# Performance work log

Hardware: AMD Instinct MI355X
Metric: run time of the kernel (lower is better)

The kernel has to match this reference:

```python
import jax, jax.numpy as jnp
import numpy as np

N_NODES = 100000
N_EDGES = 300000
HID = 256
N0, N1, N2 = 40000, 30000, 30000
D0, D1, D2 = 512, 256, 128


def setup_inputs() -> dict:
    key = jax.random.key(0)
    ks = jax.random.split(key, 14)
    s = 0.05  # init scale
    return {
        "feat0": jax.random.normal(ks[0], (N0, D0), jnp.float32),
        "feat1": jax.random.normal(ks[1], (N1, D1), jnp.float32),
        "feat2": jax.random.normal(ks[2], (N2, D2), jnp.float32),
        # per-type Linear(in_dim, HID) params (torch Linear: y = x @ W.T + b)
        "fc_w0": jax.random.normal(ks[3], (HID, D0), jnp.float32) * s,
        "fc_b0": jnp.zeros((HID,), jnp.float32),
        "fc_w1": jax.random.normal(ks[4], (HID, D1), jnp.float32) * s,
        "fc_b1": jnp.zeros((HID,), jnp.float32),
        "fc_w2": jax.random.normal(ks[5], (HID, D2), jnp.float32) * s,
        "fc_b2": jnp.zeros((HID,), jnp.float32),
        # GraphConv 1: weight=False, bias=True
        "gc1_bias": jnp.zeros((HID,), jnp.float32),
        # GraphConv 2: weight (in,out) + bias (DGL convention: feat @ W)
        "gc2_weight": jax.random.normal(ks[6], (HID, HID), jnp.float32) * s,
        "gc2_bias": jnp.zeros((HID,), jnp.float32),
        "semantic_weight": jax.random.normal(ks[7], (1, 5), jnp.float32),
        "src": jax.random.randint(ks[8], (N_EDGES,), 0, N_NODES, jnp.int64),
        "dst": jax.random.randint(ks[9], (N_EDGES,), 0, N_NODES, jnp.int64),
    }


def reference(feat0, feat1, feat2, fc_w0, fc_b0, fc_w1, fc_b1, fc_w2, fc_b2,
              gc1_bias, gc2_weight, gc2_bias, semantic_weight, src, dst):
    # per-type projection then concat along node dim -> [N_NODES, HID]
    h = jnp.concatenate([
        feat0 @ fc_w0.T + fc_b0,
        feat1 @ fc_w1.T + fc_b1,
        feat2 @ fc_w2.T + fc_b2,
    ], axis=0)

    ones = jnp.ones((src.shape[0],), h.dtype)
    deg_out = jnp.maximum(jax.ops.segment_sum(ones, src, num_segments=N_NODES), 1.0)
    deg_in = jnp.maximum(jax.ops.segment_sum(ones, dst, num_segments=N_NODES), 1.0)
    norm_out = jax.lax.rsqrt(deg_out)[:, None]  # D_out^{-1/2}
    norm_in = jax.lax.rsqrt(deg_in)[:, None]    # D_in^{-1/2}

    def gconv(x, W, b):
        # DGL GraphConv, norm='both': D_in^{-1/2} A D_out^{-1/2} x W + b, relu
        msg = (x * norm_out)[src]                                  # [E, HID]
        agg = jax.ops.segment_sum(msg, dst, num_segments=N_NODES)  # [N, HID]
        agg = agg * norm_in
        if W is not None:
            agg = agg @ W
        return jax.nn.relu(agg + b)

    # dropout is identity in eval mode
    h = gconv(h, None, gc1_bias)        # layer 0: weight=False
    h = gconv(h, gc2_weight, gc2_bias)  # layer 1
    return h, semantic_weight
```

## Files before the change

kernel.cpp:

```cpp
#include <hip/hip_runtime.h>
#include <cstdint>

#define HID 256
static constexpr int    NNODES = 100000;
static constexpr int    NEDGES = 300000;
static constexpr size_t NH     = (size_t)NNODES * HID;
static constexpr int    SCAN_B = 256;
static constexpr int    NSBLK  = (NNODES + SCAN_B - 1) / SCAN_B;

typedef __attribute__((ext_vector_type(8))) short bf16x8;
typedef __attribute__((ext_vector_type(4))) float f32x4;

__device__ __forceinline__ unsigned short f2bf(float x) {
    unsigned int u = __float_as_uint(x);
    u += 0x7fffu + ((u >> 16) & 1u);
    return (unsigned short)(u >> 16);
}
__device__ __forceinline__ unsigned int pack2(float a, float b) {
    return (unsigned int)f2bf(a) | ((unsigned int)f2bf(b) << 16);
}
__device__ __forceinline__ float bflo(unsigned int u) { return __uint_as_float(u << 16); }
__device__ __forceinline__ float bfhi(unsigned int u) { return __uint_as_float(u & 0xffff0000u); }

__global__ void zero_i32_k(int* __restrict__ p, int n) {
    int i = blockIdx.x * blockDim.x + threadIdx.x;
    if (i < n) p[i] = 0;
}

__global__ void count_deg_k(const int* __restrict__ src, const int* __restrict__ dst,
                            int* __restrict__ degout, int* __restrict__ degin) {
    int e = blockIdx.x * blockDim.x + threadIdx.x;
    if (e < NEDGES) {
        atomicAdd(degout + src[e], 1);
        atomicAdd(degin  + dst[e], 1);
    }
}

__global__ void cvt_weights_k(const float* __restrict__ w0, const float* __restrict__ w1,
                              const float* __restrict__ w2, const float* __restrict__ wg,
                              unsigned short* __restrict__ o0, unsigned short* __restrict__ o1,
                              unsigned short* __restrict__ o2, unsigned short* __restrict__ ogT) {
    int b = blockIdx.x, t = threadIdx.x;
    const float* in; unsigned short* out; int i;
    if (b < 128)      { in = w0; out = o0; i = b * 256 + t; }
    else if (b < 192) { in = w1; out = o1; i = (b - 128) * 256 + t; }
    else if (b < 224) { in = w2; out = o2; i = (b - 192) * 256 + t; }
    else {
        int n = b - 224, k = t;
        ogT[n * 256 + k] = f2bf(wg[k * 256 + n]);
        return;
    }
    float4 v = ((const float4*)in)[i];
    ushort4 w;
    w.x = f2bf(v.x); w.y = f2bf(v.y); w.z = f2bf(v.z); w.w = f2bf(v.w);
    ((ushort4*)out)[i] = w;
}

__global__ void scan_a_k(const int* __restrict__ degin, const int* __restrict__ degout,
                         int* __restrict__ row_off, int* __restrict__ bsums,
                         float* __restrict__ nout, float* __restrict__ nin,
                         const float* __restrict__ sw, float* __restrict__ tail) {
    __shared__ int sm[SCAN_B];
    int t = threadIdx.x;
    int g = blockIdx.x * SCAN_B + t;
    int v = (g < NNODES) ? degin[g] : 0;
    sm[t] = v;
    if (g < NNODES) {
        nout[g] = rsqrtf(fmaxf((float)degout[g], 1.0f));
        nin[g]  = rsqrtf(fmaxf((float)v, 1.0f));
    }
    if (g < 5) tail[g] = sw[g];
    __syncthreads();
#pragma unroll
    for (int off = 1; off < SCAN_B; off <<= 1) {
        int x = (t >= off) ? sm[t - off] : 0;
        __syncthreads();
        sm[t] += x;
        __syncthreads();
    }
    if (g < NNODES) row_off[g] = sm[t] - v;
    if (t == SCAN_B - 1) bsums[blockIdx.x] = sm[t];
}

__global__ void scan_b_k(int* __restrict__ bsums) {
    __shared__ int sm[512];
    int t = threadIdx.x;
    int v = (t < NSBLK) ? bsums[t] : 0;
    sm[t] = v;
    __syncthreads();
#pragma unroll
    for (int off = 1; off < 512; off <<= 1) {
        int x = (t >= off) ? sm[t - off] : 0;
        __syncthreads();
        sm[t] += x;
        __syncthreads();
    }
    if (t < NSBLK) bsums[t] = sm[t] - v;
}

__global__ void scan_c_k(int* __restrict__ row_off, const int* __restrict__ bsums) {
    int g = blockIdx.x * SCAN_B + threadIdx.x;
    if (g < NNODES) row_off[g] += bsums[blockIdx.x];
    if (g == 0) row_off[NNODES] = NEDGES;
}

__global__ void fill_csr_k(const int* __restrict__ src, const int* __restrict__ dst,
                           const int* __restrict__ row_off, int* __restrict__ cursor,
                           int* __restrict__ csr_src) {
    int e = blockIdx.x * blockDim.x + threadIdx.x;
    if (e < NEDGES) {
        int d = dst[e];
        int pos = row_off[d] + atomicAdd(cursor + d, 1);
        csr_src[pos] = src[e];
    }
}

template <int EPI>
__global__ __launch_bounds__(256) void gather_k(
    const unsigned short* __restrict__ h, const int* __restrict__ row_off,
    const int* __restrict__ csr_src, const float* __restrict__ nin,
    const float* __restrict__ bias, void* __restrict__ outv)
{
    int node = blockIdx.x * 4 + (threadIdx.x >> 6);
    if (node >= NNODES) return;
    int lane = threadIdx.x & 63;
    int beg = row_off[node], end = row_off[node + 1];
    float a0 = 0.f, a1 = 0.f, a2 = 0.f, a3 = 0.f;
    for (int base = beg; base < end; base += 64) {
        int cnt = end - base; if (cnt > 64) cnt = 64;
        int idx = csr_src[base + (lane < cnt ? lane : cnt - 1)];
        int j = 0;
        for (; j + 4 <= cnt; j += 4) {
            int s0 = __shfl(idx, j);
            int s1 = __shfl(idx, j + 1);
            int s2 = __shfl(idx, j + 2);
            int s3 = __shfl(idx, j + 3);
            uint2 v0 = *(const uint2*)(h + (size_t)s0 * HID + lane * 4);
            uint2 v1 = *(const uint2*)(h + (size_t)s1 * HID + lane * 4);
            uint2 v2 = *(const uint2*)(h + (size_t)s2 * HID + lane * 4);
            uint2 v3 = *(const uint2*)(h + (size_t)s3 * HID + lane * 4);
            a0 += bflo(v0.x) + bflo(v1.x) + bflo(v2.x) + bflo(v3.x);
            a1 += bfhi(v0.x) + bfhi(v1.x) + bfhi(v2.x) + bfhi(v3.x);
            a2 += bflo(v0.y) + bflo(v1.y) + bflo(v2.y) + bflo(v3.y);
            a3 += bfhi(v0.y) + bfhi(v1.y) + bfhi(v2.y) + bfhi(v3.y);
        }
        for (; j < cnt; ++j) {
            int s = __shfl(idx, j);
            uint2 v = *(const uint2*)(h + (size_t)s * HID + lane * 4);
            a0 += bflo(v.x); a1 += bfhi(v.x);
            a2 += bflo(v.y); a3 += bfhi(v.y);
        }
    }
    if (EPI) {
        float ni = nin[node];
        float4 bb = *(const float4*)(bias + lane * 4);
        float4 o;
        o.x = fmaxf(fmaf(a0, ni, bb.x), 0.f);
        o.y = fmaxf(fmaf(a1, ni, bb.y), 0.f);
        o.z = fmaxf(fmaf(a2, ni, bb.z), 0.f);
        o.w = fmaxf(fmaf(a3, ni, bb.w), 0.f);
        *(float4*)((float*)outv + (size_t)node * HID + lane * 4) = o;
    } else {
        ushort4 o;
        o.x = f2bf(a0); o.y = f2bf(a1); o.z = f2bf(a2); o.w = f2bf(a3);
        *(ushort4*)((unsigned short*)outv + (size_t)node * HID + lane * 4) = o;
    }
}

__global__ __launch_bounds__(512, 4) void proj_mfma_k(
    const float* __restrict__ f0, const float* __restrict__ f1, const float* __restrict__ f2,
    const unsigned short* __restrict__ w0, const unsigned short* __restrict__ w1,
    const unsigned short* __restrict__ w2,
    const float* __restrict__ b0, const float* __restrict__ b1, const float* __restrict__ b2,
    const float* __restrict__ nout, unsigned short* __restrict__ h0)
{
    __shared__ unsigned short As[2][128 * 32];

    int bx = blockIdx.x;
    const float* A; const unsigned short* B; const float* bias; const float* rs;
    unsigned short* C; int M, K;
    if (bx < 313)       { A = f0; B = w0; bias = b0; rs = nout;          C = h0;                          M = 40000; K = 512; }
    else if (bx < 548)  { bx -= 313; A = f1; B = w1; bias = b1; rs = nout + 40000; C = h0 + (size_t)40000 * HID; M = 30000; K = 256; }
    else                { bx -= 548; A = f2; B = w2; bias = b2; rs = nout + 70000; C = h0 + (size_t)70000 * HID; M = 30000; K = 128; }
    const int m0 = bx * 128;

    const int tid  = threadIdx.x;
    const int wid  = tid >> 6;
    const int wm   = wid >> 2;
    const int wn   = wid & 3;
    const int lane = tid & 63;
    const int half = lane >> 4;
    const int l15  = lane & 15;

    f32x4 acc[4][4];
#pragma unroll
    for (int i = 0; i < 4; ++i)
#pragma unroll
        for (int j = 0; j < 4; ++j)
#pragma unroll
            for (int r = 0; r < 4; ++r) acc[i][j][r] = 0.f;

    const int arow = tid >> 2, ac = tid & 3;
    const int aslot = ac ^ ((arow >> 1) & 3);
    int agm = m0 + arow; if (agm > M - 1) agm = M - 1;
    const float* ap = A + (size_t)agm * K + ac * 8;

    const unsigned short* bp = B + (size_t)(wn * 64 + l15 * 4) * K + half * 8;

    const int nT = K >> 5;

    float4 a0E = *(const float4*)ap;
    float4 a1E = *(const float4*)(ap + 4);
    float4 a0O = *(const float4*)(ap + 32);
    float4 a1O = *(const float4*)(ap + 36);
    bf16x8 bcur[4];

#define PROJ_STEP(P, A0, A1)                                                   \
    {                                                                          \
        uint4 u;                                                               \
        u.x = pack2(A0.x, A0.y); u.y = pack2(A0.z, A0.w);                      \
        u.z = pack2(A1.x, A1.y); u.w = pack2(A1.z, A1.w);                      \
        *(uint4*)&As[P][(arow * 4 + aslot) * 8] = u;                           \
        _Pragma("unroll")                                                      \
        for (int j = 0; j < 4; ++j)                                            \
            bcur[j] = *(const bf16x8*)(bp + (size_t)j * K + (tt + P) * 32);    \
        asm volatile("s_waitcnt lgkmcnt(0)" ::: "memory");                     \
        __builtin_amdgcn_s_barrier();                                          \
        __builtin_amdgcn_sched_barrier(0);                                     \
        {                                                                      \
            int tf = tt + P + 2; if (tf > nT - 1) tf = nT - 1;                 \
            const float* pn = ap + tf * 32;                                    \
            A0 = *(const float4*)pn; A1 = *(const float4*)(pn + 4);            \
        }                                                                      \
        bf16x8 af[4];                                                          \
        _Pragma("unroll")                                                      \
        for (int i = 0; i < 4; ++i) {                                          \
            int m = wm * 64 + i * 16 + l15;                                    \
            int ca = half ^ ((m >> 1) & 3);                                    \
            af[i] = *(const bf16x8*)&As[P][(m * 4 + ca) * 8];                  \
        }                                                                      \
        _Pragma("unroll")                                                      \
        for (int i = 0; i < 4; ++i)                                            \
            _Pragma("unroll")                                                  \
            for (int j = 0; j < 4; ++j)                                        \
                acc[i][j] = __builtin_amdgcn_mfma_f32_16x16x32_bf16(           \
                    af[i], bcur[j], acc[i][j], 0, 0, 0);                       \
    }

    for (int tt = 0; tt < nT; tt += 2) {
        PROJ_STEP(0, a0E, a1E)
        PROJ_STEP(1, a0O, a1O)
    }
#undef PROJ_STEP

    float4 bb = *(const float4*)(bias + wn * 64 + l15 * 4);
    const int mwb = m0 + wm * 64;
#pragma unroll
    for (int i = 0; i < 4; ++i) {
        int mb = mwb + i * 16 + half * 4;
        if (mb >= M) continue;
        float4 rv = *(const float4*)(rs + mb);
#pragma unroll
        for (int r = 0; r < 4; ++r) {
            float rsm = (&rv.x)[r];
            ushort4 o;
            o.x = f2bf((acc[i][0][r] + bb.x) * rsm);
            o.y = f2bf((acc[i][1][r] + bb.y) * rsm);
            o.z = f2bf((acc[i][2][r] + bb.z) * rsm);
            o.w = f2bf((acc[i][3][r] + bb.w) * rsm);
            *(ushort4*)&C[(size_t)(mb + r) * HID + wn * 64 + l15 * 4] = o;
        }
    }
}

__global__ __launch_bounds__(512, 4) void mid_mfma_k(
    const unsigned short* __restrict__ agg1, const unsigned short* __restrict__ wT,
    const float* __restrict__ b1, const float* __restrict__ nin,
    const float* __restrict__ nout, unsigned short* __restrict__ h2)
{
    __shared__ unsigned short As[2][128 * 32];

    const int m0   = blockIdx.x * 128;
    const int tid  = threadIdx.x;
    const int wid  = tid >> 6;
    const int wm   = wid >> 2;
    const int wn   = wid & 3;
    const int lane = tid & 63;
    const int half = lane >> 4;
    const int l15  = lane & 15;

    f32x4 acc[4][4];
#pragma unroll
    for (int i = 0; i < 4; ++i)
#pragma unroll
        for (int j = 0; j < 4; ++j)
#pragma unroll
            for (int r = 0; r < 4; ++r) acc[i][j][r] = 0.f;

    const int arow = tid >> 2, ac = tid & 3;
    const int aslot = ac ^ ((arow >> 1) & 3);
    int agm = m0 + arow; if (agm > NNODES - 1) agm = NNODES - 1;
    const float ni = nin[agm], no = nout[agm];
    const unsigned short* ap = agg1 + (size_t)agm * HID + ac * 8;
    const unsigned short* bp = wT + (size_t)(wn * 64 + l15 * 4) * 256 + half * 8;

    uint4  auE = *(const uint4*)ap;
    uint4  auO = *(const uint4*)(ap + 32);
    float4 cE0 = *(const float4*)(b1 + ac * 8);
    float4 cE1 = *(const float4*)(b1 + ac * 8 + 4);
    float4 cO0 = *(const float4*)(b1 + 32 + ac * 8);
    float4 cO1 = *(const float4*)(b1 + 32 + ac * 8 + 4);
    bf16x8 bcur[4];

#define MID_STEP(P, AU, C0, C1)                                                \
    {                                                                          \
        float x0 = fmaxf(fmaf(bflo(AU.x), ni, C0.x), 0.f) * no;                \
        float x1 = fmaxf(fmaf(bfhi(AU.x), ni, C0.y), 0.f) * no;                \
        float x2 = fmaxf(fmaf(bflo(AU.y), ni, C0.z), 0.f) * no;                \
        float x3 = fmaxf(fmaf(bfhi(AU.y), ni, C0.w), 0.f) * no;                \
        float x4 = fmaxf(fmaf(bflo(AU.z), ni, C1.x), 0.f) * no;                \
        float x5 = fmaxf(fmaf(bfhi(AU.z), ni, C1.y), 0.f) * no;                \
        float x6 = fmaxf(fmaf(bflo(AU.w), ni, C1.z), 0.f) * no;                \
        float x7 = fmaxf(fmaf(bfhi(AU.w), ni, C1.w), 0.f) * no;                \
        uint4 o;                                                               \
        o.x = pack2(x0, x1); o.y = pack2(x2, x3);                              \
        o.z = pack2(x4, x5); o.w = pack2(x6, x7);                              \
        *(uint4*)&As[P][(arow * 4 + aslot) * 8] = o;                           \
        _Pragma("unroll")                                                      \
        for (int j = 0; j < 4; ++j)                                            \
            bcur[j] = *(const bf16x8*)(bp + j * 256 + (tt + P) * 32);          \
        asm volatile("s_waitcnt lgkmcnt(0)" ::: "memory");                     \
        __builtin_amdgcn_s_barrier();                                          \
        __builtin_amdgcn_sched_barrier(0);                                     \
        {                                                                      \
            int tf = tt + P + 2; if (tf > 7) tf = 7;                           \
            AU = *(const uint4*)(ap + tf * 32);                                \
            C0 = *(const float4*)(b1 + tf * 32 + ac * 8);                      \
            C1 = *(const float4*)(b1 + tf * 32 + ac * 8 + 4);                  \
        }                                                                      \
        bf16x8 af[4];                                                          \
        _Pragma("unroll")                                                      \
        for (int i = 0; i < 4; ++i) {                                          \
            int m = wm * 64 + i * 16 + l15;                                    \
            int ca = half ^ ((m >> 1) & 3);                                    \
            af[i] = *(const bf16x8*)&As[P][(m * 4 + ca) * 8];                  \
        }                                                                      \
        _Pragma("unroll")                                                      \
        for (int i = 0; i < 4; ++i)                                            \
            _Pragma("unroll")                                                  \
            for (int j = 0; j < 4; ++j)                                        \
                acc[i][j] = __builtin_amdgcn_mfma_f32_16x16x32_bf16(           \
                    af[i], bcur[j], acc[i][j], 0, 0, 0);                       \
    }

    for (int tt = 0; tt < 8; tt += 2) {
        MID_STEP(0, auE, cE0, cE1)
        MID_STEP(1, auO, cO0, cO1)
    }
#undef MID_STEP

    const int mwb = m0 + wm * 64;
#pragma unroll
    for (int i = 0; i < 4; ++i) {
        int mb = mwb + i * 16 + half * 4;
        if (mb >= NNODES) continue;
#pragma unroll
        for (int r = 0; r < 4; ++r) {
            ushort4 o;
            o.x = f2bf(acc[i][0][r]);
            o.y = f2bf(acc[i][1][r]);
            o.z = f2bf(acc[i][2][r]);
            o.w = f2bf(acc[i][3][r]);
            *(ushort4*)&h2[(size_t)(mb + r) * HID + wn * 64 + l15 * 4] = o;
        }
    }
}

extern "C" void kernel_launch(void* const* d_in, const int* in_sizes, int n_in,
                              void* d_out, int out_size, void* d_ws, size_t ws_size,
                              hipStream_t stream)
{
    const float* feat0    = (const float*)d_in[0];
    const float* feat1    = (const float*)d_in[1];
    const float* feat2    = (const float*)d_in[2];
    const float* fc_w0    = (const float*)d_in[3];
    const float* fc_b0    = (const float*)d_in[4];
    const float* fc_w1    = (const float*)d_in[5];
    const float* fc_b1    = (const float*)d_in[6];
    const float* fc_w2    = (const float*)d_in[7];
    const float* fc_b2    = (const float*)d_in[8];
    const float* gc1_bias = (const float*)d_in[9];
    const float* gc2_w    = (const float*)d_in[10];
    const float* gc2_bias = (const float*)d_in[11];
    const float* sw       = (const float*)d_in[12];
    const int*   src      = (const int*)d_in[13];
    const int*   dst      = (const int*)d_in[14];

    unsigned short* h0b  = (unsigned short*)d_ws;
    unsigned short* agg1 = h0b + NH;
    unsigned short* h2b  = h0b;
    unsigned short* w0b  = agg1 + NH;
    unsigned short* w1b  = w0b + 131072;
    unsigned short* w2b  = w1b + 65536;
    unsigned short* w2Tb = w2b + 32768;
    float* nout = (float*)(w2Tb + 65536);
    float* nin  = nout + NNODES;
    int* deg_out = (int*)(nin + NNODES);
    int* deg_in  = deg_out + NNODES;
    int* cursor  = deg_in + NNODES;
    int* row_off = cursor + NNODES;
    int* bsums   = row_off + NNODES + 1;
    int* csr_src = bsums + 512;
    float* out   = (float*)d_out;

    zero_i32_k<<<(3 * NNODES + 255) / 256, 256, 0, stream>>>(deg_out, 3 * NNODES);
    cvt_weights_k<<<480, 256, 0, stream>>>(fc_w0, fc_w1, fc_w2, gc2_w,
                                           w0b, w1b, w2b, w2Tb);
    count_deg_k<<<(NEDGES + 255) / 256, 256, 0, stream>>>(src, dst, deg_out, deg_in);
    scan_a_k<<<NSBLK, SCAN_B, 0, stream>>>(deg_in, deg_out, row_off, bsums,
                                           nout, nin, sw, out + NH);
    scan_b_k<<<1, 512, 0, stream>>>(bsums);
    scan_c_k<<<NSBLK, SCAN_B, 0, stream>>>(row_off, bsums);
    fill_csr_k<<<(NEDGES + 255) / 256, 256, 0, stream>>>(src, dst, row_off, cursor, csr_src);

    proj_mfma_k<<<783, 512, 0, stream>>>(feat0, feat1, feat2, w0b, w1b, w2b,
                                         fc_b0, fc_b1, fc_b2, nout, h0b);

    gather_k<0><<<(NNODES + 3) / 4, 256, 0, stream>>>(h0b, row_off, csr_src,
                                                      nullptr, nullptr, agg1);

    mid_mfma_k<<<782, 512, 0, stream>>>(agg1, w2Tb, gc1_bias, nin, nout, h2b);

    gather_k<1><<<(NNODES + 3) / 4, 256, 0, stream>>>(h2b, row_off, csr_src,
                                                      nin, gc2_bias, out);
}
```

Measured before the change: 441.6 us.

## Shrink GEMM tiles to 64 rows, double-buffer B fragments, persistent gather

```diff
diff --git a/kernel.cpp b/kernel.cpp
--- a/kernel.cpp
+++ b/kernel.cpp
@@ -121,73 +121,83 @@
     const int* __restrict__ csr_src, const float* __restrict__ nin,
     const float* __restrict__ bias, void* __restrict__ outv)
 {
-    int node = blockIdx.x * 4 + (threadIdx.x >> 6);
-    if (node >= NNODES) return;
-    int lane = threadIdx.x & 63;
-    int beg = row_off[node], end = row_off[node + 1];
-    float a0 = 0.f, a1 = 0.f, a2 = 0.f, a3 = 0.f;
-    for (int base = beg; base < end; base += 64) {
-        int cnt = end - base; if (cnt > 64) cnt = 64;
-        int idx = csr_src[base + (lane < cnt ? lane : cnt - 1)];
-        int j = 0;
-        for (; j + 4 <= cnt; j += 4) {
-            int s0 = __shfl(idx, j);
-            int s1 = __shfl(idx, j + 1);
-            int s2 = __shfl(idx, j + 2);
-            int s3 = __shfl(idx, j + 3);
-            uint2 v0 = *(const uint2*)(h + (size_t)s0 * HID + lane * 4);
-            uint2 v1 = *(const uint2*)(h + (size_t)s1 * HID + lane * 4);
-            uint2 v2 = *(const uint2*)(h + (size_t)s2 * HID + lane * 4);
-            uint2 v3 = *(const uint2*)(h + (size_t)s3 * HID + lane * 4);
-            a0 += bflo(v0.x) + bflo(v1.x) + bflo(v2.x) + bflo(v3.x);
-            a1 += bfhi(v0.x) + bfhi(v1.x) + bfhi(v2.x) + bfhi(v3.x);
-            a2 += bflo(v0.y) + bflo(v1.y) + bflo(v2.y) + bflo(v3.y);
-            a3 += bfhi(v0.y) + bfhi(v1.y) + bfhi(v2.y) + bfhi(v3.y);
+    const int nslots = gridDim.x * 4;
+    const int wslot  = blockIdx.x * 4 + (threadIdx.x >> 6);
+    const int lane   = threadIdx.x & 63;
+    const size_t loff = (size_t)lane * 4;
+    float4 bb;
+    if (EPI) bb = *(const float4*)(bias + lane * 4);
+
+    int node = wslot;
+    int beg = 0, end = 0;
+    if (node < NNODES) { beg = row_off[node]; end = row_off[node + 1]; }
+
+    while (node < NNODES) {
+        const int nnode = node + nslots;
+        int nbeg = 0, nend = 0;
+        if (nnode < NNODES) { nbeg = row_off[nnode]; nend = row_off[nnode + 1]; }
+
+        float a0 = 0.f, a1 = 0.f, a2 = 0.f, a3 = 0.f;
+        for (int base = beg; base < end; base += 64) {
+            int cnt = end - base; if (cnt > 64) cnt = 64;
+            int idx = csr_src[base + (lane < cnt ? lane : cnt - 1)];
+            for (int j = 0; j < cnt; j += 8) {
+                uint2 v0 = {0,0}, v1 = {0,0}, v2 = {0,0}, v3 = {0,0};
+                uint2 v4 = {0,0}, v5 = {0,0}, v6 = {0,0}, v7 = {0,0};
+#define GLD(U, VU)                                                              \
+                if (j + U < cnt) {                                              \
+                    int s = __shfl(idx, j + U);                                 \
+                    VU = *(const uint2*)(h + (size_t)s * HID + loff);           \
+                }
+                GLD(0, v0) GLD(1, v1) GLD(2, v2) GLD(3, v3)
+                GLD(4, v4) GLD(5, v5) GLD(6, v6) GLD(7, v7)
+#undef GLD
+                a0 += (bflo(v0.x) + bflo(v1.x)) + (bflo(v2.x) + bflo(v3.x))
+                    + (bflo(v4.x) + bflo(v5.x)) + (bflo(v6.x) + bflo(v7.x));
+                a1 += (bfhi(v0.x) + bfhi(v1.x)) + (bfhi(v2.x) + bfhi(v3.x))
+                    + (bfhi(v4.x) + bfhi(v5.x)) + (bfhi(v6.x) + bfhi(v7.x));
+                a2 += (bflo(v0.y) + bflo(v1.y)) + (bflo(v2.y) + bflo(v3.y))
+                    + (bflo(v4.y) + bflo(v5.y)) + (bflo(v6.y) + bflo(v7.y));
+                a3 += (bfhi(v0.y) + bfhi(v1.y)) + (bfhi(v2.y) + bfhi(v3.y))
+                    + (bfhi(v4.y) + bfhi(v5.y)) + (bfhi(v6.y) + bfhi(v7.y));
+            }
         }
-        for (; j < cnt; ++j) {
-            int s = __shfl(idx, j);
-            uint2 v = *(const uint2*)(h + (size_t)s * HID + lane * 4);
-            a0 += bflo(v.x); a1 += bfhi(v.x);
-            a2 += bflo(v.y); a3 += bfhi(v.y);
+        if (EPI) {
+            float ni = nin[node];
+            float4 o;
+            o.x = fmaxf(fmaf(a0, ni, bb.x), 0.f);
+            o.y = fmaxf(fmaf(a1, ni, bb.y), 0.f);
+            o.z = fmaxf(fmaf(a2, ni, bb.z), 0.f);
+            o.w = fmaxf(fmaf(a3, ni, bb.w), 0.f);
+            *(float4*)((float*)outv + (size_t)node * HID + lane * 4) = o;
+        } else {
+            ushort4 o;
+            o.x = f2bf(a0); o.y = f2bf(a1); o.z = f2bf(a2); o.w = f2bf(a3);
+            *(ushort4*)((unsigned short*)outv + (size_t)node * HID + lane * 4) = o;
         }
-    }
-    if (EPI) {
-        float ni = nin[node];
-        float4 bb = *(const float4*)(bias + lane * 4);
-        float4 o;
-        o.x = fmaxf(fmaf(a0, ni, bb.x), 0.f);
-        o.y = fmaxf(fmaf(a1, ni, bb.y), 0.f);
-        o.z = fmaxf(fmaf(a2, ni, bb.z), 0.f);
-        o.w = fmaxf(fmaf(a3, ni, bb.w), 0.f);
-        *(float4*)((float*)outv + (size_t)node * HID + lane * 4) = o;
-    } else {
-        ushort4 o;
-        o.x = f2bf(a0); o.y = f2bf(a1); o.z = f2bf(a2); o.w = f2bf(a3);
-        *(ushort4*)((unsigned short*)outv + (size_t)node * HID + lane * 4) = o;
-    }
-}
-
-__global__ __launch_bounds__(512, 4) void proj_mfma_k(
+        node = nnode; beg = nbeg; end = nend;
+    }
+}
+
+__global__ __launch_bounds__(256, 3) void proj_mfma_k(
     const float* __restrict__ f0, const float* __restrict__ f1, const float* __restrict__ f2,
     const unsigned short* __restrict__ w0, const unsigned short* __restrict__ w1,
     const unsigned short* __restrict__ w2,
     const float* __restrict__ b0, const float* __restrict__ b1, const float* __restrict__ b2,
     const float* __restrict__ nout, unsigned short* __restrict__ h0)
 {
-    __shared__ unsigned short As[2][128 * 32];
+    __shared__ unsigned short As[2][64 * 32];
 
     int bx = blockIdx.x;
     const float* A; const unsigned short* B; const float* bias; const float* rs;
     unsigned short* C; int M, K;
-    if (bx < 313)       { A = f0; B = w0; bias = b0; rs = nout;          C = h0;                          M = 40000; K = 512; }
-    else if (bx < 548)  { bx -= 313; A = f1; B = w1; bias = b1; rs = nout + 40000; C = h0 + (size_t)40000 * HID; M = 30000; K = 256; }
-    else                { bx -= 548; A = f2; B = w2; bias = b2; rs = nout + 70000; C = h0 + (size_t)70000 * HID; M = 30000; K = 128; }
-    const int m0 = bx * 128;
+    if (bx < 625)       { A = f0; B = w0; bias = b0; rs = nout;          C = h0;                          M = 40000; K = 512; }
+    else if (bx < 1094) { bx -= 625;  A = f1; B = w1; bias = b1; rs = nout + 40000; C = h0 + (size_t)40000 * HID; M = 30000; K = 256; }
+    else                { bx -= 1094; A = f2; B = w2; bias = b2; rs = nout + 70000; C = h0 + (size_t)70000 * HID; M = 30000; K = 128; }
+    const int m0 = bx * 64;
 
     const int tid  = threadIdx.x;
-    const int wid  = tid >> 6;
-    const int wm   = wid >> 2;
-    const int wn   = wid & 3;
+    const int wn   = tid >> 6;
     const int lane = tid & 63;
     const int half = lane >> 4;
     const int l15  = lane & 15;
@@ -209,13 +219,15 @@
 
     const int nT = K >> 5;
 
-    float4 a0E = *(const float4*)ap;
-    float4 a1E = *(const float4*)(ap + 4);
-    float4 a0O = *(const float4*)(ap + 32);
-    float4 a1O = *(const float4*)(ap + 36);
-    bf16x8 bcur[4];
-
-#define PROJ_STEP(P, A0, A1)                                                   \
+    float4 aE0 = *(const float4*)ap;
+    float4 aE1 = *(const float4*)(ap + 4);
+    float4 aO0 = *(const float4*)(ap + 32);
+    float4 aO1 = *(const float4*)(ap + 36);
+    bf16x8 bE[4], bO[4];
+#pragma unroll
+    for (int j = 0; j < 4; ++j) bE[j] = *(const bf16x8*)(bp + (size_t)j * K);
+
+#define PROJ_STEP(P, A0, A1, BC, BN, TB, TF)                                   \
     {                                                                          \
         uint4 u;                                                               \
         u.x = pack2(A0.x, A0.y); u.y = pack2(A0.z, A0.w);                      \
@@ -223,19 +235,19 @@
         *(uint4*)&As[P][(arow * 4 + aslot) * 8] = u;                           \
         _Pragma("unroll")                                                      \
         for (int j = 0; j < 4; ++j)                                            \
-            bcur[j] = *(const bf16x8*)(bp + (size_t)j * K + (tt + P) * 32);    \
+            BN[j] = *(const bf16x8*)(bp + (size_t)j * K + (TB) * 32);          \
         asm volatile("s_waitcnt lgkmcnt(0)" ::: "memory");                     \
         __builtin_amdgcn_s_barrier();                                          \
+        asm volatile("" ::: "memory");                                         \
         __builtin_amdgcn_sched_barrier(0);                                     \
         {                                                                      \
-            int tf = tt + P + 2; if (tf > nT - 1) tf = nT - 1;                 \
-            const float* pn = ap + tf * 32;                                    \
+            const float* pn = ap + (TF) * 32;                                  \
             A0 = *(const float4*)pn; A1 = *(const float4*)(pn + 4);            \
         }                                                                      \
         bf16x8 af[4];                                                          \
         _Pragma("unroll")                                                      \
         for (int i = 0; i < 4; ++i) {                                          \
-            int m = wm * 64 + i * 16 + l15;                                    \
+            int m = i * 16 + l15;                                              \
             int ca = half ^ ((m >> 1) & 3);                                    \
             af[i] = *(const bf16x8*)&As[P][(m * 4 + ca) * 8];                  \
         }                                                                      \
@@ -244,20 +256,23 @@
             _Pragma("unroll")                                                  \
             for (int j = 0; j < 4; ++j)                                        \
                 acc[i][j] = __builtin_amdgcn_mfma_f32_16x16x32_bf16(           \
-                    af[i], bcur[j], acc[i][j], 0, 0, 0);                       \
-    }
-
-    for (int tt = 0; tt < nT; tt += 2) {
-        PROJ_STEP(0, a0E, a1E)
-        PROJ_STEP(1, a0O, a1O)
+                    af[i], BC[j], acc[i][j], 0, 0, 0);                         \
+    }
+
+    for (int t = 0; t < nT; t += 2) {
+        const int tb0 = t + 1;
+        const int tf0 = (t + 2 < nT) ? t + 2 : nT - 1;
+        PROJ_STEP(0, aE0, aE1, bE, bO, tb0, tf0)
+        const int tb1 = (t + 2 < nT) ? t + 2 : nT - 1;
+        const int tf1 = (t + 3 < nT) ? t + 3 : nT - 1;
+        PROJ_STEP(1, aO0, aO1, bO, bE, tb1, tf1)
     }
 #undef PROJ_STEP
 
     float4 bb = *(const float4*)(bias + wn * 64 + l15 * 4);
-    const int mwb = m0 + wm * 64;
 #pragma unroll
     for (int i = 0; i < 4; ++i) {
-        int mb = mwb + i * 16 + half * 4;
+        int mb = m0 + i * 16 + half * 4;
         if (mb >= M) continue;
         float4 rv = *(const float4*)(rs + mb);
 #pragma unroll
@@ -273,18 +288,16 @@
     }
 }
 
-__global__ __launch_bounds__(512, 4) void mid_mfma_k(
+__global__ __launch_bounds__(256, 3) void mid_mfma_k(
     const unsigned short* __restrict__ agg1, const unsigned short* __restrict__ wT,
     const float* __restrict__ b1, const float* __restrict__ nin,
     const float* __restrict__ nout, unsigned short* __restrict__ h2)
 {
-    __shared__ unsigned short As[2][128 * 32];
-
-    const int m0   = blockIdx.x * 128;
+    __shared__ unsigned short As[2][64 * 32];
+
+    const int m0   = blockIdx.x * 64;
     const int tid  = threadIdx.x;
-    const int wid  = tid >> 6;
-    const int wm   = wid >> 2;
-    const int wn   = wid & 3;
+    const int wn   = tid >> 6;
     const int lane = tid & 63;
     const int half = lane >> 4;
     const int l15  = lane & 15;
@@ -310,9 +323,11 @@
     float4 cE1 = *(const float4*)(b1 + ac * 8 + 4);
     float4 cO0 = *(const float4*)(b1 + 32 + ac * 8);
     float4 cO1 = *(const float4*)(b1 + 32 + ac * 8 + 4);
-    bf16x8 bcur[4];
-
-#define MID_STEP(P, AU, C0, C1)                                                \
+    bf16x8 bE[4], bO[4];
+#pragma unroll
+    for (int j = 0; j < 4; ++j) bE[j] = *(const bf16x8*)(bp + (size_t)j * 256);
+
+#define MID_STEP(P, AU, C0, C1, BC, BN, TB, TF)                                \
     {                                                                          \
         float x0 = fmaxf(fmaf(bflo(AU.x), ni, C0.x), 0.f) * no;                \
         float x1 = fmaxf(fmaf(bfhi(AU.x), ni, C0.y), 0.f) * no;                \
@@ -328,20 +343,20 @@
         *(uint4*)&As[P][(arow * 4 + aslot) * 8] = o;                           \
         _Pragma("unroll")                                                      \
         for (int j = 0; j < 4; ++j)                                            \
-            bcur[j] = *(const bf16x8*)(bp + j * 256 + (tt + P) * 32);          \
+            BN[j] = *(const bf16x8*)(bp + (size_t)j * 256 + (TB) * 32);        \
         asm volatile("s_waitcnt lgkmcnt(0)" ::: "memory");                     \
         __builtin_amdgcn_s_barrier();                                          \
+        asm volatile("" ::: "memory");                                         \
         __builtin_amdgcn_sched_barrier(0);                                     \
         {                                                                      \
-            int tf = tt + P + 2; if (tf > 7) tf = 7;                           \
-            AU = *(const uint4*)(ap + tf * 32);                                \
-            C0 = *(const float4*)(b1 + tf * 32 + ac * 8);                      \
-            C1 = *(const float4*)(b1 + tf * 32 + ac * 8 + 4);                  \
+            AU = *(const uint4*)(ap + (TF) * 32);                              \
+            C0 = *(const float4*)(b1 + (TF) * 32 + ac * 8);                    \
+            C1 = *(const float4*)(b1 + (TF) * 32 + ac * 8 + 4);                \
         }                                                                      \
         bf16x8 af[4];                                                          \
         _Pragma("unroll")                                                      \
         for (int i = 0; i < 4; ++i) {                                          \
-            int m = wm * 64 + i * 16 + l15;                                    \
+            int m = i * 16 + l15;                                              \
             int ca = half ^ ((m >> 1) & 3);                                    \
             af[i] = *(const bf16x8*)&As[P][(m * 4 + ca) * 8];                  \
         }                                                                      \
@@ -350,19 +365,22 @@
             _Pragma("unroll")                                                  \
             for (int j = 0; j < 4; ++j)                                        \
                 acc[i][j] = __builtin_amdgcn_mfma_f32_16x16x32_bf16(           \
-                    af[i], bcur[j], acc[i][j], 0, 0, 0);                       \
-    }
-
-    for (int tt = 0; tt < 8; tt += 2) {
-        MID_STEP(0, auE, cE0, cE1)
-        MID_STEP(1, auO, cO0, cO1)
+                    af[i], BC[j], acc[i][j], 0, 0, 0);                         \
+    }
+
+    for (int t = 0; t < 8; t += 2) {
+        const int tb0 = t + 1;
+        const int tf0 = (t + 2 < 8) ? t + 2 : 7;
+        MID_STEP(0, auE, cE0, cE1, bE, bO, tb0, tf0)
+        const int tb1 = (t + 2 < 8) ? t + 2 : 7;
+        const int tf1 = (t + 3 < 8) ? t + 3 : 7;
+        MID_STEP(1, auO, cO0, cO1, bO, bE, tb1, tf1)
     }
 #undef MID_STEP
 
-    const int mwb = m0 + wm * 64;
 #pragma unroll
     for (int i = 0; i < 4; ++i) {
-        int mb = mwb + i * 16 + half * 4;
+        int mb = m0 + i * 16 + half * 4;
         if (mb >= NNODES) continue;
 #pragma unroll
         for (int r = 0; r < 4; ++r) {
@@ -423,14 +441,14 @@
     scan_c_k<<<NSBLK, SCAN_B, 0, stream>>>(row_off, bsums);
     fill_csr_k<<<(NEDGES + 255) / 256, 256, 0, stream>>>(src, dst, row_off, cursor, csr_src);
 
-    proj_mfma_k<<<783, 512, 0, stream>>>(feat0, feat1, feat2, w0b, w1b, w2b,
-                                         fc_b0, fc_b1, fc_b2, nout, h0b);
-
-    gather_k<0><<<(NNODES + 3) / 4, 256, 0, stream>>>(h0b, row_off, csr_src,
-                                                      nullptr, nullptr, agg1);
-
-    mid_mfma_k<<<782, 512, 0, stream>>>(agg1, w2Tb, gc1_bias, nin, nout, h2b);
-
-    gather_k<1><<<(NNODES + 3) / 4, 256, 0, stream>>>(h2b, row_off, csr_src,
-                                                      nin, gc2_bias, out);
-}
+    proj_mfma_k<<<1563, 256, 0, stream>>>(feat0, feat1, feat2, w0b, w1b, w2b,
+                                          fc_b0, fc_b1, fc_b2, nout, h0b);
+
+    gather_k<0><<<2048, 256, 0, stream>>>(h0b, row_off, csr_src,
+                                          nullptr, nullptr, agg1);
+
+    mid_mfma_k<<<1563, 256, 0, stream>>>(agg1, w2Tb, gc1_bias, nin, nout, h2b);
+
+    gather_k<1><<<2048, 256, 0, stream>>>(h2b, row_off, csr_src,
+                                          nin, gc2_bias, out);
+}
```

Result: faster. 416.4 us (-5.7%).
